# Performance work log

Measured on AMD Instinct MI355X. Metric: run time of the kernel, lower is better.

Reference implementation:

```python
import jax, jax.numpy as jnp
import numpy as np

N = 4096
D_IN = 1024
D_OUT = 1024
NUM_HEADS = 16
HEAD_DIM = D_OUT // NUM_HEADS


def setup_inputs() -> dict:
    key = jax.random.key(0)
    ks = jax.random.split(key, 7)
    scale = 1.0 / np.sqrt(D_IN)
    return {
        "q": jax.random.normal(ks[0], (N, D_IN), dtype=jnp.float32),
        "k": jax.random.normal(ks[1], (N, D_IN), dtype=jnp.float32),
        "v": jax.random.normal(ks[2], (N, D_IN), dtype=jnp.float32),
        "W_q": jax.random.normal(ks[3], (D_IN, D_OUT), dtype=jnp.float32) * scale,
        "W_k": jax.random.normal(ks[4], (D_IN, D_OUT), dtype=jnp.float32) * scale,
        "W_v": jax.random.normal(ks[5], (D_IN, D_OUT), dtype=jnp.float32) * scale,
        "W_o": jax.random.normal(ks[6], (D_OUT, D_OUT), dtype=jnp.float32) * scale,
    }


def reference(q, k, v, W_q, W_k, W_v, W_o):
    n = q.shape[0]
    # QKV projections -> [h, n, d]
    Q = (q @ W_q).reshape(n, NUM_HEADS, HEAD_DIM).transpose(1, 0, 2)
    K = (k @ W_k).reshape(n, NUM_HEADS, HEAD_DIM).transpose(1, 0, 2)
    V = (v @ W_v).reshape(n, NUM_HEADS, HEAD_DIM).transpose(1, 0, 2)
    scores = jnp.einsum('hid,hjd->hij', Q, K) / jnp.sqrt(jnp.float32(HEAD_DIM))
    attn = jax.nn.softmax(scores, axis=-1)  # dropout p=0.0 (eval) -> no-op
    h = jnp.einsum('hij,hjd->hid', attn, V)
    h = h.transpose(1, 0, 2).reshape(n, D_OUT)
    return h @ W_o
```

## Files before the change

kernel.cpp:

```cpp
#include <hip/hip_runtime.h>
#include <math.h>

#define NTOK   4096
#define DMODEL 1024
#define NHEADS 16
#define HDIM   64
#define KDIM   1024

typedef __attribute__((ext_vector_type(8))) short          bf16x8;
typedef __attribute__((ext_vector_type(4))) float          f32x4;
typedef __attribute__((ext_vector_type(4))) unsigned short us4;

static __device__ __forceinline__ unsigned short f2bf(float f) {
    unsigned int u = __float_as_uint(f);
    u += 0x7fffu + ((u >> 16) & 1u);
    return (unsigned short)(u >> 16);
}

static __device__ __forceinline__ unsigned int pk2bf(float a, float b) {
#if __has_builtin(__builtin_amdgcn_cvt_pk_bf16_f32)
    return __builtin_bit_cast(unsigned int,
                              __builtin_amdgcn_cvt_pk_bf16_f32(a, b));
#else
    unsigned int ua = __float_as_uint(a) + 0x8000u;
    unsigned int ub = __float_as_uint(b) + 0x8000u;
    return __builtin_amdgcn_perm(ub, ua, 0x07060302u);
#endif
}

#if __has_builtin(__builtin_amdgcn_exp2f)
#define EXP2(x) __builtin_amdgcn_exp2f(x)
#else
#define EXP2(x) exp2f(x)
#endif

static __device__ __forceinline__ void async_copy16(void* lds, const void* g) {
    __builtin_amdgcn_global_load_lds(
        (const __attribute__((address_space(1))) unsigned int*)g,
        (__attribute__((address_space(3))) unsigned int*)lds, 16, 0, 0);
}

__global__ __launch_bounds__(256)
void cast_wt_kernel(const float* __restrict__ Wq, const float* __restrict__ Wk,
                    const float* __restrict__ Wv, const float* __restrict__ Wo,
                    unsigned short* __restrict__ Tq, unsigned short* __restrict__ Tk,
                    unsigned short* __restrict__ Tv, unsigned short* __restrict__ To) {
    __shared__ float Ws[64][65];
    const float* W;
    unsigned short* T;
    switch (blockIdx.z) {
        case 0:  W = Wq; T = Tq; break;
        case 1:  W = Wk; T = Tk; break;
        case 2:  W = Wv; T = Tv; break;
        default: W = Wo; T = To; break;
    }
    const int k0 = blockIdx.x * 64, n0 = blockIdx.y * 64;
    const int t = threadIdx.x;
    #pragma unroll
    for (int i = 0; i < 4; i++) {
        int c  = i * 256 + t;
        int kk = c >> 4;
        int n4 = (c & 15) << 2;
        *(float4*)(&Ws[kk][n4]) =
            *(const float4*)(W + (size_t)(k0 + kk) * DMODEL + n0 + n4);
    }
    __syncthreads();
    #pragma unroll
    for (int i = 0; i < 4; i++) {
        int c  = i * 256 + t;
        int nn = c >> 4;
        int k4 = (c & 15) << 2;
        us4 o = { f2bf(Ws[k4 + 0][nn]), f2bf(Ws[k4 + 1][nn]),
                  f2bf(Ws[k4 + 2][nn]), f2bf(Ws[k4 + 3][nn]) };
        *(us4*)(T + (size_t)(n0 + nn) * KDIM + k0 + k4) = o;
    }
}

__global__ __launch_bounds__(256)
void cast_in_kernel(const float* __restrict__ q, const float* __restrict__ k,
                    const float* __restrict__ v,
                    unsigned short* __restrict__ Qb,
                    unsigned short* __restrict__ Kb,
                    unsigned short* __restrict__ Vb) {
    const float* src;
    unsigned short* dst;
    switch (blockIdx.y) {
        case 0:  src = q; dst = Qb; break;
        case 1:  src = k; dst = Kb; break;
        default: src = v; dst = Vb; break;
    }
    size_t i = ((size_t)blockIdx.x * 256 + threadIdx.x) * 8;
    float4 f0 = *(const float4*)(src + i);
    float4 f1 = *(const float4*)(src + i + 4);
    uint2 o0 = { pk2bf(f0.x, f0.y), pk2bf(f0.z, f0.w) };
    uint2 o1 = { pk2bf(f1.x, f1.y), pk2bf(f1.z, f1.w) };
    *(uint2*)(dst + i)     = o0;
    *(uint2*)(dst + i + 4) = o1;
}

__global__ __launch_bounds__(256, 3)
void qkv_gemm_pre(const unsigned short* __restrict__ Qb,
                  const unsigned short* __restrict__ Kb,
                  const unsigned short* __restrict__ Vb,
                  const unsigned short* __restrict__ Btq,
                  const unsigned short* __restrict__ Btk,
                  const unsigned short* __restrict__ Btv,
                  unsigned short* __restrict__ Oq, unsigned short* __restrict__ Ok,
                  unsigned short* __restrict__ Ov) {
    __shared__ unsigned short As[128 * 64];
    __shared__ unsigned short Bs[128 * 64];

    const unsigned short* A;
    const unsigned short* Bt;
    unsigned short* Out;
    int mode;
    float sc;
    switch (blockIdx.z) {
        case 0:  A = Qb; Bt = Btq; Out = Oq; mode = 1; sc = 0.18033688011112042f; break;
        case 1:  A = Kb; Bt = Btk; Out = Ok; mode = 1; sc = 1.0f; break;
        default: A = Vb; Bt = Btv; Out = Ov; mode = 2; sc = 1.0f; break;
    }

    const int t    = threadIdx.x;
    const int w    = t >> 6;
    const int lane = t & 63;
    const int quad = lane >> 4;
    const int l15  = lane & 15;
    const int wr   = w >> 1, wc = w & 1;
    const int bm   = blockIdx.y * 128, bn = blockIdx.x * 128;

    f32x4 acc[4][4];
    #pragma unroll
    for (int i = 0; i < 4; i++)
        #pragma unroll
        for (int j = 0; j < 4; j++) acc[i][j] = (f32x4)(0.f);

    for (int k0 = 0; k0 < KDIM; k0 += 64) {
        __syncthreads();
        #pragma unroll
        for (int i = 0; i < 4; i++) {
            int cb = (i * 4 + w) * 64;
            int c  = cb + lane;
            int r  = c >> 3;
            int ko = (c & 7) * 8;
            async_copy16((void*)(Bs + cb * 8),
                         (const void*)(Bt + (size_t)(bn + r) * KDIM + k0 + ko));
            async_copy16((void*)(As + cb * 8),
                         (const void*)(A + (size_t)(bm + r) * KDIM + k0 + ko));
        }
        __syncthreads();
        #pragma unroll
        for (int kq = 0; kq < 2; kq++) {
            bf16x8 af[4], bf[4];
            #pragma unroll
            for (int mt = 0; mt < 4; mt++)
                af[mt] = *(bf16x8*)(As + (wr * 64 + mt * 16 + l15) * 64 + kq * 32 + quad * 8);
            #pragma unroll
            for (int nt = 0; nt < 4; nt++)
                bf[nt] = *(bf16x8*)(Bs + (wc * 64 + nt * 16 + l15) * 64 + kq * 32 + quad * 8);
            #pragma unroll
            for (int mt = 0; mt < 4; mt++)
                #pragma unroll
                for (int nt = 0; nt < 4; nt++)
                    acc[mt][nt] = __builtin_amdgcn_mfma_f32_16x16x32_bf16(
                        af[mt], bf[nt], acc[mt][nt], 0, 0, 0);
        }
    }

    #pragma unroll
    for (int mt = 0; mt < 4; mt++) {
        #pragma unroll
        for (int nt = 0; nt < 4; nt++) {
            int col  = bn + wc * 64 + nt * 16 + l15;
            int row0 = bm + wr * 64 + mt * 16 + quad * 4;
            if (mode == 1) {
                size_t base = ((size_t)(col >> 6)) * NTOK * HDIM + (col & 63);
                #pragma unroll
                for (int r = 0; r < 4; r++)
                    Out[base + (size_t)(row0 + r) * HDIM] = f2bf(acc[mt][nt][r] * sc);
            } else {
                size_t base = ((size_t)(col >> 6)) * HDIM * NTOK +
                              (size_t)(col & 63) * NTOK + row0;
                us4 o = { f2bf(acc[mt][nt][0]), f2bf(acc[mt][nt][1]),
                          f2bf(acc[mt][nt][2]), f2bf(acc[mt][nt][3]) };
                *(us4*)(Out + base) = o;
            }
        }
    }
}

__global__ __launch_bounds__(256, 3)
void qkv_gemm(const float* __restrict__ Aq, const float* __restrict__ Ak,
              const float* __restrict__ Av,
              const unsigned short* __restrict__ Btq,
              const unsigned short* __restrict__ Btk,
              const unsigned short* __restrict__ Btv,
              unsigned short* __restrict__ Oq, unsigned short* __restrict__ Ok,
              unsigned short* __restrict__ Ov) {
    __shared__ unsigned short As[128 * 64];
    __shared__ unsigned short Bs[128 * 64];

    const float* A;
    const unsigned short* Bt;
    unsigned short* Out;
    int mode;
    float sc;
    switch (blockIdx.z) {
        case 0:  A = Aq; Bt = Btq; Out = Oq; mode = 1; sc = 0.18033688011112042f; break;
        case 1:  A = Ak; Bt = Btk; Out = Ok; mode = 1; sc = 1.0f; break;
        default: A = Av; Bt = Btv; Out = Ov; mode = 2; sc = 1.0f; break;
    }

    const int t    = threadIdx.x;
    const int w    = t >> 6;
    const int lane = t & 63;
    const int quad = lane >> 4;
    const int l15  = lane & 15;
    const int wr   = w >> 1, wc = w & 1;
    const int bm   = blockIdx.y * 128, bn = blockIdx.x * 128;

    f32x4 acc[4][4];
    #pragma unroll
    for (int i = 0; i < 4; i++)
        #pragma unroll
        for (int j = 0; j < 4; j++) acc[i][j] = (f32x4)(0.f);

    for (int k0 = 0; k0 < KDIM; k0 += 64) {
        __syncthreads();
        #pragma unroll
        for (int i = 0; i < 4; i++) {
            int cb = (i * 4 + w) * 64;
            int c  = cb + lane;
            int r  = c >> 3;
            int ko = (c & 7) * 8;
            async_copy16((void*)(Bs + cb * 8),
                         (const void*)(Bt + (size_t)(bn + r) * KDIM + k0 + ko));
        }
        #pragma unroll
        for (int i = 0; i < 4; i++) {
            int c2 = i * 256 + t;
            int r  = c2 >> 3;
            int k8 = (c2 & 7) * 8;
            const float* src = A + (size_t)(bm + r) * KDIM + k0 + k8;
            float4 f0 = *(const float4*)(src);
            float4 f1 = *(const float4*)(src + 4);
            uint2 p0 = { pk2bf(f0.x, f0.y), pk2bf(f0.z, f0.w) };
            uint2 p1 = { pk2bf(f1.x, f1.y), pk2bf(f1.z, f1.w) };
            *(uint2*)(As + r * 64 + k8)     = p0;
            *(uint2*)(As + r * 64 + k8 + 4) = p1;
        }
        __syncthreads();
        #pragma unroll
        for (int kq = 0; kq < 2; kq++) {
            bf16x8 af[4], bf[4];
            #pragma unroll
            for (int mt = 0; mt < 4; mt++)
                af[mt] = *(bf16x8*)(As + (wr * 64 + mt * 16 + l15) * 64 + kq * 32 + quad * 8);
            #pragma unroll
            for (int nt = 0; nt < 4; nt++)
                bf[nt] = *(bf16x8*)(Bs + (wc * 64 + nt * 16 + l15) * 64 + kq * 32 + quad * 8);
            #pragma unroll
            for (int mt = 0; mt < 4; mt++)
                #pragma unroll
                for (int nt = 0; nt < 4; nt++)
                    acc[mt][nt] = __builtin_amdgcn_mfma_f32_16x16x32_bf16(
                        af[mt], bf[nt], acc[mt][nt], 0, 0, 0);
        }
    }

    #pragma unroll
    for (int mt = 0; mt < 4; mt++) {
        #pragma unroll
        for (int nt = 0; nt < 4; nt++) {
            int col  = bn + wc * 64 + nt * 16 + l15;
            int row0 = bm + wr * 64 + mt * 16 + quad * 4;
            if (mode == 1) {
                size_t base = ((size_t)(col >> 6)) * NTOK * HDIM + (col & 63);
                #pragma unroll
                for (int r = 0; r < 4; r++)
                    Out[base + (size_t)(row0 + r) * HDIM] = f2bf(acc[mt][nt][r] * sc);
            } else {
                size_t base = ((size_t)(col >> 6)) * HDIM * NTOK +
                              (size_t)(col & 63) * NTOK + row0;
                us4 o = { f2bf(acc[mt][nt][0]), f2bf(acc[mt][nt][1]),
                          f2bf(acc[mt][nt][2]), f2bf(acc[mt][nt][3]) };
                *(us4*)(Out + base) = o;
            }
        }
    }
}

__global__ __launch_bounds__(256, 3)
void out_gemm(const unsigned short* __restrict__ A,
              const unsigned short* __restrict__ Bt,
              float* __restrict__ Out) {
    __shared__ unsigned short As[128 * 64];
    __shared__ unsigned short Bs[128 * 64];

    const int t    = threadIdx.x;
    const int w    = t >> 6;
    const int lane = t & 63;
    const int quad = lane >> 4;
    const int l15  = lane & 15;
    const int wr   = w >> 1, wc = w & 1;
    const int bm   = blockIdx.y * 128, bn = blockIdx.x * 128;

    f32x4 acc[4][4];
    #pragma unroll
    for (int i = 0; i < 4; i++)
        #pragma unroll
        for (int j = 0; j < 4; j++) acc[i][j] = (f32x4)(0.f);

    for (int k0 = 0; k0 < KDIM; k0 += 64) {
        __syncthreads();
        #pragma unroll
        for (int i = 0; i < 4; i++) {
            int cb = (i * 4 + w) * 64;
            int c  = cb + lane;
            int r  = c >> 3;
            int ko = (c & 7) * 8;
            async_copy16((void*)(Bs + cb * 8),
                         (const void*)(Bt + (size_t)(bn + r) * KDIM + k0 + ko));
            async_copy16((void*)(As + cb * 8),
                         (const void*)(A + (size_t)(bm + r) * KDIM + k0 + ko));
        }
        __syncthreads();
        #pragma unroll
        for (int kq = 0; kq < 2; kq++) {
            bf16x8 af[4], bf[4];
            #pragma unroll
            for (int mt = 0; mt < 4; mt++)
                af[mt] = *(bf16x8*)(As + (wr * 64 + mt * 16 + l15) * 64 + kq * 32 + quad * 8);
            #pragma unroll
            for (int nt = 0; nt < 4; nt++)
                bf[nt] = *(bf16x8*)(Bs + (wc * 64 + nt * 16 + l15) * 64 + kq * 32 + quad * 8);
            #pragma unroll
            for (int mt = 0; mt < 4; mt++)
                #pragma unroll
                for (int nt = 0; nt < 4; nt++)
                    acc[mt][nt] = __builtin_amdgcn_mfma_f32_16x16x32_bf16(
                        af[mt], bf[nt], acc[mt][nt], 0, 0, 0);
        }
    }

    #pragma unroll
    for (int mt = 0; mt < 4; mt++) {
        #pragma unroll
        for (int nt = 0; nt < 4; nt++) {
            int col  = bn + wc * 64 + nt * 16 + l15;
            int row0 = bm + wr * 64 + mt * 16 + quad * 4;
            #pragma unroll
            for (int r = 0; r < 4; r++)
                Out[(size_t)(row0 + r) * DMODEL + col] = acc[mt][nt][r];
        }
    }
}

__global__ __launch_bounds__(256)
void attn_mfma(const unsigned short* __restrict__ Q,
               const unsigned short* __restrict__ K,
               const unsigned short* __restrict__ Vt,
               unsigned short* __restrict__ ctx) {
    __shared__ __align__(16) unsigned short Ks[2 * 4096];
    __shared__ __align__(16) unsigned short Vs[2 * 4096];
    __shared__ __align__(16) unsigned short Ps[4][32][72];

    const int h    = blockIdx.y;
    const int qt   = blockIdx.x;
    const int t    = threadIdx.x;
    const int w    = t >> 6;
    const int lane = t & 63;
    const int quad = lane >> 4;
    const int l15  = lane & 15;

    const unsigned short* Qg =
        Q + ((size_t)h * NTOK + qt * 128 + w * 32 + l15) * HDIM;
    bf16x8 qf[2][2];
    qf[0][0] = *(const bf16x8*)(Qg + quad * 8);
    qf[0][1] = *(const bf16x8*)(Qg + 32 + quad * 8);
    qf[1][0] = *(const bf16x8*)(Qg + 16 * HDIM + quad * 8);
    qf[1][1] = *(const bf16x8*)(Qg + 16 * HDIM + 32 + quad * 8);

    const unsigned short* Kg = K  + (size_t)h * NTOK * HDIM;
    const unsigned short* Vg = Vt + (size_t)h * HDIM * NTOK;

    const int rr = t >> 3;
    const int oo = ((t & 7) ^ (rr & 7)) * 8;
    const unsigned short* kbase = Kg + (size_t)rr * HDIM + oo;
    const unsigned short* vbase = Vg + (size_t)rr * NTOK + oo;
    unsigned short* ksd = Ks + w * 512;
    unsigned short* vsd = Vs + w * 512;

    auto stage = [&](int kt, int b) {
        const unsigned short* kp = kbase + (size_t)kt * 64 * HDIM;
        const unsigned short* vp = vbase + kt * 64;
        async_copy16((void*)(ksd + b * 4096),        (const void*)kp);
        async_copy16((void*)(ksd + b * 4096 + 2048), (const void*)(kp + 32 * HDIM));
        async_copy16((void*)(vsd + b * 4096),        (const void*)vp);
        async_copy16((void*)(vsd + b * 4096 + 2048), (const void*)(vp + (size_t)32 * NTOK));
    };

    const int xb = l15 & 7;
    const int a0 = l15 * 64 + ((quad    ) ^ xb) * 8;
    const int a1 = l15 * 64 + ((quad + 4) ^ xb) * 8;

    const bf16x8 ones = { 16256, 16256, 16256, 16256,
                          16256, 16256, 16256, 16256 };

    f32x4 O[2][4];
    f32x4 lacc[2];
    #pragma unroll
    for (int tl = 0; tl < 2; tl++) {
        lacc[tl] = (f32x4)(0.f);
        #pragma unroll
        for (int dt = 0; dt < 4; dt++) O[tl][dt] = (f32x4)(0.f);
    }

    stage(0, 0);

    for (int kt = 0; kt < NTOK / 64; kt++) {
        const int cur = kt & 1;
        __syncthreads();
        if (kt + 1 < NTOK / 64) stage(kt + 1, cur ^ 1);

        f32x4 s[2][4];
        #pragma unroll
        for (int kc = 0; kc < 4; kc++) {
            bf16x8 kf0 = *(bf16x8*)(Ks + cur * 4096 + kc * 1024 + a0);
            bf16x8 kf1 = *(bf16x8*)(Ks + cur * 4096 + kc * 1024 + a1);
            #pragma unroll
            for (int tl = 0; tl < 2; tl++) {
                f32x4 acc = (f32x4)(0.f);
                acc = __builtin_amdgcn_mfma_f32_16x16x32_bf16(kf0, qf[tl][0], acc, 0, 0, 0);
                acc = __builtin_amdgcn_mfma_f32_16x16x32_bf16(kf1, qf[tl][1], acc, 0, 0, 0);
                s[tl][kc] = acc;
            }
        }

        bf16x8 vf[4][2];
        #pragma unroll
        for (int dt = 0; dt < 4; dt++) {
            vf[dt][0] = *(bf16x8*)(Vs + cur * 4096 + dt * 1024 + a0);
            vf[dt][1] = *(bf16x8*)(Vs + cur * 4096 + dt * 1024 + a1);
        }

        #pragma unroll
        for (int tl = 0; tl < 2; tl++) {
            #pragma unroll
            for (int kc = 0; kc < 4; kc++) {
                float e0 = EXP2(s[tl][kc][0]);
                float e1 = EXP2(s[tl][kc][1]);
                float e2 = EXP2(s[tl][kc][2]);
                float e3 = EXP2(s[tl][kc][3]);
                uint2 p = { pk2bf(e0, e1), pk2bf(e2, e3) };
                *(uint2*)(&Ps[w][tl * 16 + l15][kc * 16 + quad * 4]) = p;
            }
            asm volatile("s_waitcnt lgkmcnt(0)" ::: "memory");

            bf16x8 pf0 = *(bf16x8*)(&Ps[w][tl * 16 + l15][quad * 8]);
            bf16x8 pf1 = *(bf16x8*)(&Ps[w][tl * 16 + l15][32 + quad * 8]);
            lacc[tl] = __builtin_amdgcn_mfma_f32_16x16x32_bf16(ones, pf0, lacc[tl], 0, 0, 0);
            lacc[tl] = __builtin_amdgcn_mfma_f32_16x16x32_bf16(ones, pf1, lacc[tl], 0, 0, 0);
            #pragma unroll
            for (int dt = 0; dt < 4; dt++) {
                O[tl][dt] = __builtin_amdgcn_mfma_f32_16x16x32_bf16(vf[dt][0], pf0, O[tl][dt], 0, 0, 0);
                O[tl][dt] = __builtin_amdgcn_mfma_f32_16x16x32_bf16(vf[dt][1], pf1, O[tl][dt], 0, 0, 0);
            }
        }
    }

    #pragma unroll
    for (int tl = 0; tl < 2; tl++) {
        float inv = 1.f / lacc[tl][0];
        size_t row = (size_t)qt * 128 + w * 32 + tl * 16 + l15;
        #pragma unroll
        for (int dt = 0; dt < 4; dt++) {
            uint2 o = { pk2bf(O[tl][dt][0] * inv, O[tl][dt][1] * inv),
                        pk2bf(O[tl][dt][2] * inv, O[tl][dt][3] * inv) };
            *(uint2*)(ctx + row * DMODEL + h * HDIM + dt * 16 + quad * 4) = o;
        }
    }
}

extern "C" void kernel_launch(void* const* d_in, const int* in_sizes, int n_in,
                              void* d_out, int out_size, void* d_ws, size_t ws_size,
                              hipStream_t stream) {
    const float* q  = (const float*)d_in[0];
    const float* k  = (const float*)d_in[1];
    const float* v  = (const float*)d_in[2];
    const float* Wq = (const float*)d_in[3];
    const float* Wk = (const float*)d_in[4];
    const float* Wv = (const float*)d_in[5];
    const float* Wo = (const float*)d_in[6];
    float* out = (float*)d_out;

    unsigned short* WqT = (unsigned short*)d_ws;
    unsigned short* WkT = WqT + (size_t)DMODEL * KDIM;
    unsigned short* WvT = WkT + (size_t)DMODEL * KDIM;
    unsigned short* WoT = WvT + (size_t)DMODEL * KDIM;
    unsigned short* Qh  = WoT + (size_t)DMODEL * KDIM;
    unsigned short* Kh  = Qh  + (size_t)NTOK * DMODEL;
    unsigned short* Vth = Kh  + (size_t)NTOK * DMODEL;
    unsigned short* ctx = Vth + (size_t)NTOK * DMODEL;
    unsigned short* Qb  = ctx + (size_t)NTOK * DMODEL;
    unsigned short* Kb  = Qb  + (size_t)NTOK * DMODEL;
    unsigned short* Vb  = Kb  + (size_t)NTOK * DMODEL;

    const bool precast = ws_size >= (size_t)67108864;

    cast_wt_kernel<<<dim3(16, 16, 4), 256, 0, stream>>>(Wq, Wk, Wv, Wo,
                                                        WqT, WkT, WvT, WoT);
    if (precast) {
        cast_in_kernel<<<dim3(2048, 3), 256, 0, stream>>>(q, k, v, Qb, Kb, Vb);
        qkv_gemm_pre<<<dim3(DMODEL / 128, NTOK / 128, 3), 256, 0, stream>>>(
            Qb, Kb, Vb, WqT, WkT, WvT, Qh, Kh, Vth);
    } else {
        qkv_gemm<<<dim3(DMODEL / 128, NTOK / 128, 3), 256, 0, stream>>>(
            q, k, v, WqT, WkT, WvT, Qh, Kh, Vth);
    }
    attn_mfma<<<dim3(NTOK / 128, NHEADS), 256, 0, stream>>>(Qh, Kh, Vth, ctx);
    out_gemm<<<dim3(DMODEL / 128, NTOK / 128), 256, 0, stream>>>(ctx, WoT, out);
}
```

Before: 277.4 us.

## Load attention K/V fragments directly from global memory and shrink tiles

The attention kernel stops staging K and V tiles through double-buffered shared memory and reads MFMA fragments straight from global (relying on L2/L1 reuse across blocks). Each block now covers 64 query rows instead of 128, with a flattened, head-interleaved grid and occupancy hint 4, so there are more concurrent blocks. The output GEMM tile is halved in M to double its block count. This removes LDS staging and barriers, but every wave now reloads K/V from cache without any intra-block sharing, which increases global/L2 traffic and exposes load latency with no prefetch.

```diff
diff --git a/kernel.cpp b/kernel.cpp
--- a/kernel.cpp
+++ b/kernel.cpp
@@ -294,7 +294,7 @@
 void out_gemm(const unsigned short* __restrict__ A,
               const unsigned short* __restrict__ Bt,
               float* __restrict__ Out) {
-    __shared__ unsigned short As[128 * 64];
+    __shared__ unsigned short As[64 * 64];
     __shared__ unsigned short Bs[128 * 64];
 
     const int t    = threadIdx.x;
@@ -303,11 +303,11 @@
     const int quad = lane >> 4;
     const int l15  = lane & 15;
     const int wr   = w >> 1, wc = w & 1;
-    const int bm   = blockIdx.y * 128, bn = blockIdx.x * 128;
-
-    f32x4 acc[4][4];
-    #pragma unroll
-    for (int i = 0; i < 4; i++)
+    const int bm   = blockIdx.y * 64, bn = blockIdx.x * 128;
+
+    f32x4 acc[2][4];
+    #pragma unroll
+    for (int i = 0; i < 2; i++)
         #pragma unroll
         for (int j = 0; j < 4; j++) acc[i][j] = (f32x4)(0.f);
 
@@ -321,21 +321,28 @@
             int ko = (c & 7) * 8;
             async_copy16((void*)(Bs + cb * 8),
                          (const void*)(Bt + (size_t)(bn + r) * KDIM + k0 + ko));
+        }
+        #pragma unroll
+        for (int i = 0; i < 2; i++) {
+            int cb = (i * 4 + w) * 64;
+            int c  = cb + lane;
+            int r  = c >> 3;
+            int ko = (c & 7) * 8;
             async_copy16((void*)(As + cb * 8),
                          (const void*)(A + (size_t)(bm + r) * KDIM + k0 + ko));
         }
         __syncthreads();
         #pragma unroll
         for (int kq = 0; kq < 2; kq++) {
-            bf16x8 af[4], bf[4];
-            #pragma unroll
-            for (int mt = 0; mt < 4; mt++)
-                af[mt] = *(bf16x8*)(As + (wr * 64 + mt * 16 + l15) * 64 + kq * 32 + quad * 8);
+            bf16x8 af[2], bf[4];
+            #pragma unroll
+            for (int mt = 0; mt < 2; mt++)
+                af[mt] = *(bf16x8*)(As + (wr * 32 + mt * 16 + l15) * 64 + kq * 32 + quad * 8);
             #pragma unroll
             for (int nt = 0; nt < 4; nt++)
                 bf[nt] = *(bf16x8*)(Bs + (wc * 64 + nt * 16 + l15) * 64 + kq * 32 + quad * 8);
             #pragma unroll
-            for (int mt = 0; mt < 4; mt++)
+            for (int mt = 0; mt < 2; mt++)
                 #pragma unroll
                 for (int nt = 0; nt < 4; nt++)
                     acc[mt][nt] = __builtin_amdgcn_mfma_f32_16x16x32_bf16(
@@ -344,11 +351,11 @@
     }
 
     #pragma unroll
-    for (int mt = 0; mt < 4; mt++) {
+    for (int mt = 0; mt < 2; mt++) {
         #pragma unroll
         for (int nt = 0; nt < 4; nt++) {
             int col  = bn + wc * 64 + nt * 16 + l15;
-            int row0 = bm + wr * 64 + mt * 16 + quad * 4;
+            int row0 = bm + wr * 32 + mt * 16 + quad * 4;
             #pragma unroll
             for (int r = 0; r < 4; r++)
                 Out[(size_t)(row0 + r) * DMODEL + col] = acc[mt][nt][r];
@@ -356,17 +363,16 @@
     }
 }
 
-__global__ __launch_bounds__(256)
+__global__ __launch_bounds__(256, 4)
 void attn_mfma(const unsigned short* __restrict__ Q,
                const unsigned short* __restrict__ K,
                const unsigned short* __restrict__ Vt,
                unsigned short* __restrict__ ctx) {
-    __shared__ __align__(16) unsigned short Ks[2 * 4096];
-    __shared__ __align__(16) unsigned short Vs[2 * 4096];
-    __shared__ __align__(16) unsigned short Ps[4][32][72];
-
-    const int h    = blockIdx.y;
-    const int qt   = blockIdx.x;
+    __shared__ __align__(16) unsigned short Ps[4][16][72];
+
+    const int bid  = blockIdx.x;
+    const int h    = bid & 15;
+    const int qt   = bid >> 4;
     const int t    = threadIdx.x;
     const int w    = t >> 6;
     const int lane = t & 63;
@@ -374,111 +380,94 @@
     const int l15  = lane & 15;
 
     const unsigned short* Qg =
-        Q + ((size_t)h * NTOK + qt * 128 + w * 32 + l15) * HDIM;
-    bf16x8 qf[2][2];
-    qf[0][0] = *(const bf16x8*)(Qg + quad * 8);
-    qf[0][1] = *(const bf16x8*)(Qg + 32 + quad * 8);
-    qf[1][0] = *(const bf16x8*)(Qg + 16 * HDIM + quad * 8);
-    qf[1][1] = *(const bf16x8*)(Qg + 16 * HDIM + 32 + quad * 8);
-
-    const unsigned short* Kg = K  + (size_t)h * NTOK * HDIM;
-    const unsigned short* Vg = Vt + (size_t)h * HDIM * NTOK;
-
-    const int rr = t >> 3;
-    const int oo = ((t & 7) ^ (rr & 7)) * 8;
-    const unsigned short* kbase = Kg + (size_t)rr * HDIM + oo;
-    const unsigned short* vbase = Vg + (size_t)rr * NTOK + oo;
-    unsigned short* ksd = Ks + w * 512;
-    unsigned short* vsd = Vs + w * 512;
-
-    auto stage = [&](int kt, int b) {
-        const unsigned short* kp = kbase + (size_t)kt * 64 * HDIM;
-        const unsigned short* vp = vbase + kt * 64;
-        async_copy16((void*)(ksd + b * 4096),        (const void*)kp);
-        async_copy16((void*)(ksd + b * 4096 + 2048), (const void*)(kp + 32 * HDIM));
-        async_copy16((void*)(vsd + b * 4096),        (const void*)vp);
-        async_copy16((void*)(vsd + b * 4096 + 2048), (const void*)(vp + (size_t)32 * NTOK));
-    };
-
-    const int xb = l15 & 7;
-    const int a0 = l15 * 64 + ((quad    ) ^ xb) * 8;
-    const int a1 = l15 * 64 + ((quad + 4) ^ xb) * 8;
+        Q + ((size_t)h * NTOK + qt * 64 + w * 16 + l15) * HDIM;
+    bf16x8 qf0 = *(const bf16x8*)(Qg + quad * 8);
+    bf16x8 qf1 = *(const bf16x8*)(Qg + 32 + quad * 8);
+
+    const unsigned short* kp0 = K + ((size_t)h * NTOK + l15) * HDIM + quad * 8;
+    const unsigned short* kp1 = kp0 + 32 * HDIM;
+    const unsigned short* vp0 = Vt + ((size_t)h * HDIM + l15) * NTOK + quad * 8;
+    const unsigned short* vp1 = vp0 + (size_t)16 * NTOK;
+    const unsigned short* vp2 = vp0 + (size_t)32 * NTOK;
+    const unsigned short* vp3 = vp0 + (size_t)48 * NTOK;
 
     const bf16x8 ones = { 16256, 16256, 16256, 16256,
                           16256, 16256, 16256, 16256 };
 
-    f32x4 O[2][4];
-    f32x4 lacc[2];
-    #pragma unroll
-    for (int tl = 0; tl < 2; tl++) {
-        lacc[tl] = (f32x4)(0.f);
-        #pragma unroll
-        for (int dt = 0; dt < 4; dt++) O[tl][dt] = (f32x4)(0.f);
-    }
-
-    stage(0, 0);
+    f32x4 O[4];
+    f32x4 lacc = (f32x4)(0.f);
+    #pragma unroll
+    for (int dt = 0; dt < 4; dt++) O[dt] = (f32x4)(0.f);
 
     for (int kt = 0; kt < NTOK / 64; kt++) {
-        const int cur = kt & 1;
-        __syncthreads();
-        if (kt + 1 < NTOK / 64) stage(kt + 1, cur ^ 1);
-
-        f32x4 s[2][4];
+        f32x4 s[4];
+        {
+            bf16x8 kf00 = *(const bf16x8*)(kp0);
+            bf16x8 kf01 = *(const bf16x8*)(kp0 + 32);
+            bf16x8 kf10 = *(const bf16x8*)(kp0 + 16 * HDIM);
+            bf16x8 kf11 = *(const bf16x8*)(kp0 + 16 * HDIM + 32);
+            bf16x8 kf20 = *(const bf16x8*)(kp1);
+            bf16x8 kf21 = *(const bf16x8*)(kp1 + 32);
+            bf16x8 kf30 = *(const bf16x8*)(kp1 + 16 * HDIM);
+            bf16x8 kf31 = *(const bf16x8*)(kp1 + 16 * HDIM + 32);
+            f32x4 a0 = (f32x4)(0.f), a1 = (f32x4)(0.f),
+                  a2 = (f32x4)(0.f), a3 = (f32x4)(0.f);
+            a0 = __builtin_amdgcn_mfma_f32_16x16x32_bf16(kf00, qf0, a0, 0, 0, 0);
+            a1 = __builtin_amdgcn_mfma_f32_16x16x32_bf16(kf10, qf0, a1, 0, 0, 0);
+            a2 = __builtin_amdgcn_mfma_f32_16x16x32_bf16(kf20, qf0, a2, 0, 0, 0);
+            a3 = __builtin_amdgcn_mfma_f32_16x16x32_bf16(kf30, qf0, a3, 0, 0, 0);
+            a0 = __builtin_amdgcn_mfma_f32_16x16x32_bf16(kf01, qf1, a0, 0, 0, 0);
+            a1 = __builtin_amdgcn_mfma_f32_16x16x32_bf16(kf11, qf1, a1, 0, 0, 0);
+            a2 = __builtin_amdgcn_mfma_f32_16x16x32_bf16(kf21, qf1, a2, 0, 0, 0);
+            a3 = __builtin_amdgcn_mfma_f32_16x16x32_bf16(kf31, qf1, a3, 0, 0, 0);
+            s[0] = a0; s[1] = a1; s[2] = a2; s[3] = a3;
+        }
+        kp0 += 64 * HDIM;
+        kp1 += 64 * HDIM;
+
+        bf16x8 vf00 = *(const bf16x8*)(vp0);
+        bf16x8 vf01 = *(const bf16x8*)(vp0 + 32);
+        bf16x8 vf10 = *(const bf16x8*)(vp1);
+        bf16x8 vf11 = *(const bf16x8*)(vp1 + 32);
+        bf16x8 vf20 = *(const bf16x8*)(vp2);
+        bf16x8 vf21 = *(const bf16x8*)(vp2 + 32);
+        bf16x8 vf30 = *(const bf16x8*)(vp3);
+        bf16x8 vf31 = *(const bf16x8*)(vp3 + 32);
+        vp0 += 64; vp1 += 64; vp2 += 64; vp3 += 64;
+
         #pragma unroll
         for (int kc = 0; kc < 4; kc++) {
-            bf16x8 kf0 = *(bf16x8*)(Ks + cur * 4096 + kc * 1024 + a0);
-            bf16x8 kf1 = *(bf16x8*)(Ks + cur * 4096 + kc * 1024 + a1);
-            #pragma unroll
-            for (int tl = 0; tl < 2; tl++) {
-                f32x4 acc = (f32x4)(0.f);
-                acc = __builtin_amdgcn_mfma_f32_16x16x32_bf16(kf0, qf[tl][0], acc, 0, 0, 0);
-                acc = __builtin_amdgcn_mfma_f32_16x16x32_bf16(kf1, qf[tl][1], acc, 0, 0, 0);
-                s[tl][kc] = acc;
-            }
-        }
-
-        bf16x8 vf[4][2];
-        #pragma unroll
-        for (int dt = 0; dt < 4; dt++) {
-            vf[dt][0] = *(bf16x8*)(Vs + cur * 4096 + dt * 1024 + a0);
-            vf[dt][1] = *(bf16x8*)(Vs + cur * 4096 + dt * 1024 + a1);
-        }
-
-        #pragma unroll
-        for (int tl = 0; tl < 2; tl++) {
-            #pragma unroll
-            for (int kc = 0; kc < 4; kc++) {
-                float e0 = EXP2(s[tl][kc][0]);
-                float e1 = EXP2(s[tl][kc][1]);
-                float e2 = EXP2(s[tl][kc][2]);
-                float e3 = EXP2(s[tl][kc][3]);
-                uint2 p = { pk2bf(e0, e1), pk2bf(e2, e3) };
-                *(uint2*)(&Ps[w][tl * 16 + l15][kc * 16 + quad * 4]) = p;
-            }
-            asm volatile("s_waitcnt lgkmcnt(0)" ::: "memory");
-
-            bf16x8 pf0 = *(bf16x8*)(&Ps[w][tl * 16 + l15][quad * 8]);
-            bf16x8 pf1 = *(bf16x8*)(&Ps[w][tl * 16 + l15][32 + quad * 8]);
-            lacc[tl] = __builtin_amdgcn_mfma_f32_16x16x32_bf16(ones, pf0, lacc[tl], 0, 0, 0);
-            lacc[tl] = __builtin_amdgcn_mfma_f32_16x16x32_bf16(ones, pf1, lacc[tl], 0, 0, 0);
-            #pragma unroll
-            for (int dt = 0; dt < 4; dt++) {
-                O[tl][dt] = __builtin_amdgcn_mfma_f32_16x16x32_bf16(vf[dt][0], pf0, O[tl][dt], 0, 0, 0);
-                O[tl][dt] = __builtin_amdgcn_mfma_f32_16x16x32_bf16(vf[dt][1], pf1, O[tl][dt], 0, 0, 0);
-            }
-        }
-    }
-
-    #pragma unroll
-    for (int tl = 0; tl < 2; tl++) {
-        float inv = 1.f / lacc[tl][0];
-        size_t row = (size_t)qt * 128 + w * 32 + tl * 16 + l15;
-        #pragma unroll
-        for (int dt = 0; dt < 4; dt++) {
-            uint2 o = { pk2bf(O[tl][dt][0] * inv, O[tl][dt][1] * inv),
-                        pk2bf(O[tl][dt][2] * inv, O[tl][dt][3] * inv) };
-            *(uint2*)(ctx + row * DMODEL + h * HDIM + dt * 16 + quad * 4) = o;
-        }
+            float e0 = EXP2(s[kc][0]);
+            float e1 = EXP2(s[kc][1]);
+            float e2 = EXP2(s[kc][2]);
+            float e3 = EXP2(s[kc][3]);
+            uint2 p = { pk2bf(e0, e1), pk2bf(e2, e3) };
+            *(uint2*)(&Ps[w][l15][kc * 16 + quad * 4]) = p;
+        }
+        asm volatile("s_waitcnt lgkmcnt(0)" ::: "memory");
+
+        bf16x8 pf0 = *(bf16x8*)(&Ps[w][l15][quad * 8]);
+        bf16x8 pf1 = *(bf16x8*)(&Ps[w][l15][32 + quad * 8]);
+
+        lacc  = __builtin_amdgcn_mfma_f32_16x16x32_bf16(ones, pf0, lacc, 0, 0, 0);
+        O[0]  = __builtin_amdgcn_mfma_f32_16x16x32_bf16(vf00, pf0, O[0], 0, 0, 0);
+        O[1]  = __builtin_amdgcn_mfma_f32_16x16x32_bf16(vf10, pf0, O[1], 0, 0, 0);
+        O[2]  = __builtin_amdgcn_mfma_f32_16x16x32_bf16(vf20, pf0, O[2], 0, 0, 0);
+        O[3]  = __builtin_amdgcn_mfma_f32_16x16x32_bf16(vf30, pf0, O[3], 0, 0, 0);
+        lacc  = __builtin_amdgcn_mfma_f32_16x16x32_bf16(ones, pf1, lacc, 0, 0, 0);
+        O[0]  = __builtin_amdgcn_mfma_f32_16x16x32_bf16(vf01, pf1, O[0], 0, 0, 0);
+        O[1]  = __builtin_amdgcn_mfma_f32_16x16x32_bf16(vf11, pf1, O[1], 0, 0, 0);
+        O[2]  = __builtin_amdgcn_mfma_f32_16x16x32_bf16(vf21, pf1, O[2], 0, 0, 0);
+        O[3]  = __builtin_amdgcn_mfma_f32_16x16x32_bf16(vf31, pf1, O[3], 0, 0, 0);
+    }
+
+    float inv = 1.f / lacc[0];
+    size_t row = (size_t)qt * 64 + w * 16 + l15;
+    #pragma unroll
+    for (int dt = 0; dt < 4; dt++) {
+        uint2 o = { pk2bf(O[dt][0] * inv, O[dt][1] * inv),
+                    pk2bf(O[dt][2] * inv, O[dt][3] * inv) };
+        *(uint2*)(ctx + row * DMODEL + h * HDIM + dt * 16 + quad * 4) = o;
     }
 }
 
@@ -518,6 +507,6 @@
         qkv_gemm<<<dim3(DMODEL / 128, NTOK / 128, 3), 256, 0, stream>>>(
             q, k, v, WqT, WkT, WvT, Qh, Kh, Vth);
     }
-    attn_mfma<<<dim3(NTOK / 128, NHEADS), 256, 0, stream>>>(Qh, Kh, Vth, ctx);
-    out_gemm<<<dim3(DMODEL / 128, NTOK / 128), 256, 0, stream>>>(ctx, WoT, out);
-}
+    attn_mfma<<<dim3(NTOK / 64 * NHEADS), 256, 0, stream>>>(Qh, Kh, Vth, ctx);
+    out_gemm<<<dim3(DMODEL / 128, NTOK / 64), 256, 0, stream>>>(ctx, WoT, out);
+}
```

Measured after the change: 611.6 us. 2.2x slower.

## Split attention KV range across two blocks with combine pass; shrink out_gemm M-tile

Applied to the files above, without the earlier changes.

Attention is split along the key dimension into two halves, each computed by its own block. Each half writes unnormalized bf16 partial outputs and row sums, and a separate combine kernel adds the halves and normalizes. This doubles the number of attention blocks to improve CU occupancy, at the cost of extra global traffic and one more launch. The output GEMM tile is reduced from 128 to 64 rows, doubling its grid for better load balance at the price of less B-tile reuse.

```diff
diff --git a/kernel.cpp b/kernel.cpp
--- a/kernel.cpp
+++ b/kernel.cpp
@@ -294,7 +294,7 @@
 void out_gemm(const unsigned short* __restrict__ A,
               const unsigned short* __restrict__ Bt,
               float* __restrict__ Out) {
-    __shared__ unsigned short As[128 * 64];
+    __shared__ unsigned short As[64 * 64];
     __shared__ unsigned short Bs[128 * 64];
 
     const int t    = threadIdx.x;
@@ -303,11 +303,11 @@
     const int quad = lane >> 4;
     const int l15  = lane & 15;
     const int wr   = w >> 1, wc = w & 1;
-    const int bm   = blockIdx.y * 128, bn = blockIdx.x * 128;
-
-    f32x4 acc[4][4];
-    #pragma unroll
-    for (int i = 0; i < 4; i++)
+    const int bm   = blockIdx.y * 64, bn = blockIdx.x * 128;
+
+    f32x4 acc[2][4];
+    #pragma unroll
+    for (int i = 0; i < 2; i++)
         #pragma unroll
         for (int j = 0; j < 4; j++) acc[i][j] = (f32x4)(0.f);
 
@@ -321,21 +321,28 @@
             int ko = (c & 7) * 8;
             async_copy16((void*)(Bs + cb * 8),
                          (const void*)(Bt + (size_t)(bn + r) * KDIM + k0 + ko));
+        }
+        #pragma unroll
+        for (int i = 0; i < 2; i++) {
+            int cb = (i * 4 + w) * 64;
+            int c  = cb + lane;
+            int r  = c >> 3;
+            int ko = (c & 7) * 8;
             async_copy16((void*)(As + cb * 8),
                          (const void*)(A + (size_t)(bm + r) * KDIM + k0 + ko));
         }
         __syncthreads();
         #pragma unroll
         for (int kq = 0; kq < 2; kq++) {
-            bf16x8 af[4], bf[4];
-            #pragma unroll
-            for (int mt = 0; mt < 4; mt++)
-                af[mt] = *(bf16x8*)(As + (wr * 64 + mt * 16 + l15) * 64 + kq * 32 + quad * 8);
+            bf16x8 af[2], bf[4];
+            #pragma unroll
+            for (int mt = 0; mt < 2; mt++)
+                af[mt] = *(bf16x8*)(As + (wr * 32 + mt * 16 + l15) * 64 + kq * 32 + quad * 8);
             #pragma unroll
             for (int nt = 0; nt < 4; nt++)
                 bf[nt] = *(bf16x8*)(Bs + (wc * 64 + nt * 16 + l15) * 64 + kq * 32 + quad * 8);
             #pragma unroll
-            for (int mt = 0; mt < 4; mt++)
+            for (int mt = 0; mt < 2; mt++)
                 #pragma unroll
                 for (int nt = 0; nt < 4; nt++)
                     acc[mt][nt] = __builtin_amdgcn_mfma_f32_16x16x32_bf16(
@@ -344,16 +351,166 @@
     }
 
     #pragma unroll
-    for (int mt = 0; mt < 4; mt++) {
+    for (int mt = 0; mt < 2; mt++) {
         #pragma unroll
         for (int nt = 0; nt < 4; nt++) {
             int col  = bn + wc * 64 + nt * 16 + l15;
-            int row0 = bm + wr * 64 + mt * 16 + quad * 4;
+            int row0 = bm + wr * 32 + mt * 16 + quad * 4;
             #pragma unroll
             for (int r = 0; r < 4; r++)
                 Out[(size_t)(row0 + r) * DMODEL + col] = acc[mt][nt][r];
         }
     }
+}
+
+__global__ __launch_bounds__(256, 4)
+void attn_split(const unsigned short* __restrict__ Q,
+                const unsigned short* __restrict__ K,
+                const unsigned short* __restrict__ Vt,
+                unsigned short* __restrict__ PO,
+                float* __restrict__ lbuf) {
+    __shared__ __align__(16) unsigned short Ks[4096];
+    __shared__ __align__(16) unsigned short Vs[4096];
+    __shared__ __align__(16) unsigned short Ps[4][16][72];
+
+    const int qt   = blockIdx.x;
+    const int h    = blockIdx.y;
+    const int half = blockIdx.z;
+    const int t    = threadIdx.x;
+    const int w    = t >> 6;
+    const int lane = t & 63;
+    const int quad = lane >> 4;
+    const int l15  = lane & 15;
+
+    const unsigned short* Qg =
+        Q + ((size_t)h * NTOK + qt * 128 + w * 32 + l15) * HDIM;
+    bf16x8 qf[2][2];
+    qf[0][0] = *(const bf16x8*)(Qg + quad * 8);
+    qf[0][1] = *(const bf16x8*)(Qg + 32 + quad * 8);
+    qf[1][0] = *(const bf16x8*)(Qg + 16 * HDIM + quad * 8);
+    qf[1][1] = *(const bf16x8*)(Qg + 16 * HDIM + 32 + quad * 8);
+
+    const unsigned short* Kg = K  + ((size_t)h * NTOK + half * 2048) * HDIM;
+    const unsigned short* Vg = Vt + (size_t)h * HDIM * NTOK + half * 2048;
+
+    const int rr = t >> 3;
+    const int oo = ((t & 7) ^ (rr & 7)) * 8;
+    const unsigned short* kbase = Kg + (size_t)rr * HDIM + oo;
+    const unsigned short* vbase = Vg + (size_t)rr * NTOK + oo;
+    unsigned short* ksd = Ks + w * 512;
+    unsigned short* vsd = Vs + w * 512;
+
+    const int xb = l15 & 7;
+    const int a0 = l15 * 64 + ((quad    ) ^ xb) * 8;
+    const int a1 = l15 * 64 + ((quad + 4) ^ xb) * 8;
+
+    const bf16x8 ones = { 16256, 16256, 16256, 16256,
+                          16256, 16256, 16256, 16256 };
+
+    f32x4 O[2][4];
+    f32x4 lacc[2];
+    #pragma unroll
+    for (int tl = 0; tl < 2; tl++) {
+        lacc[tl] = (f32x4)(0.f);
+        #pragma unroll
+        for (int dt = 0; dt < 4; dt++) O[tl][dt] = (f32x4)(0.f);
+    }
+
+    for (int kt = 0; kt < 32; kt++) {
+        __syncthreads();
+        {
+            const unsigned short* kp = kbase + (size_t)kt * 64 * HDIM;
+            const unsigned short* vp = vbase + kt * 64;
+            async_copy16((void*)(ksd),        (const void*)kp);
+            async_copy16((void*)(ksd + 2048), (const void*)(kp + 32 * HDIM));
+            async_copy16((void*)(vsd),        (const void*)vp);
+            async_copy16((void*)(vsd + 2048), (const void*)(vp + (size_t)32 * NTOK));
+        }
+        __syncthreads();
+
+        f32x4 s[2][4];
+        #pragma unroll
+        for (int kc = 0; kc < 4; kc++) {
+            bf16x8 kf0 = *(bf16x8*)(Ks + kc * 1024 + a0);
+            bf16x8 kf1 = *(bf16x8*)(Ks + kc * 1024 + a1);
+            #pragma unroll
+            for (int tl = 0; tl < 2; tl++) {
+                f32x4 acc = (f32x4)(0.f);
+                acc = __builtin_amdgcn_mfma_f32_16x16x32_bf16(kf0, qf[tl][0], acc, 0, 0, 0);
+                acc = __builtin_amdgcn_mfma_f32_16x16x32_bf16(kf1, qf[tl][1], acc, 0, 0, 0);
+                s[tl][kc] = acc;
+            }
+        }
+
+        bf16x8 vf[4][2];
+        #pragma unroll
+        for (int dt = 0; dt < 4; dt++) {
+            vf[dt][0] = *(bf16x8*)(Vs + dt * 1024 + a0);
+            vf[dt][1] = *(bf16x8*)(Vs + dt * 1024 + a1);
+        }
+
+        #pragma unroll
+        for (int tl = 0; tl < 2; tl++) {
+            #pragma unroll
+            for (int kc = 0; kc < 4; kc++) {
+                float e0 = EXP2(s[tl][kc][0]);
+                float e1 = EXP2(s[tl][kc][1]);
+                float e2 = EXP2(s[tl][kc][2]);
+                float e3 = EXP2(s[tl][kc][3]);
+                uint2 p = { pk2bf(e0, e1), pk2bf(e2, e3) };
+                *(uint2*)(&Ps[w][l15][kc * 16 + quad * 4]) = p;
+            }
+            asm volatile("s_waitcnt lgkmcnt(0)" ::: "memory");
+
+            bf16x8 pf0 = *(bf16x8*)(&Ps[w][l15][quad * 8]);
+            bf16x8 pf1 = *(bf16x8*)(&Ps[w][l15][32 + quad * 8]);
+            lacc[tl] = __builtin_amdgcn_mfma_f32_16x16x32_bf16(ones, pf0, lacc[tl], 0, 0, 0);
+            lacc[tl] = __builtin_amdgcn_mfma_f32_16x16x32_bf16(ones, pf1, lacc[tl], 0, 0, 0);
+            #pragma unroll
+            for (int dt = 0; dt < 4; dt++) {
+                O[tl][dt] = __builtin_amdgcn_mfma_f32_16x16x32_bf16(vf[dt][0], pf0, O[tl][dt], 0, 0, 0);
+                O[tl][dt] = __builtin_amdgcn_mfma_f32_16x16x32_bf16(vf[dt][1], pf1, O[tl][dt], 0, 0, 0);
+            }
+        }
+    }
+
+    unsigned short* POh = PO + (size_t)half * NTOK * DMODEL;
+    #pragma unroll
+    for (int tl = 0; tl < 2; tl++) {
+        size_t row = (size_t)qt * 128 + w * 32 + tl * 16 + l15;
+        #pragma unroll
+        for (int dt = 0; dt < 4; dt++) {
+            uint2 o = { pk2bf(O[tl][dt][0], O[tl][dt][1]),
+                        pk2bf(O[tl][dt][2], O[tl][dt][3]) };
+            *(uint2*)(POh + row * DMODEL + h * HDIM + dt * 16 + quad * 4) = o;
+        }
+        if (quad == 0)
+            lbuf[((size_t)half * NHEADS + h) * NTOK + row] = lacc[tl][0];
+    }
+}
+
+__global__ __launch_bounds__(256)
+void combine_kernel(const unsigned short* __restrict__ PO,
+                    const float* __restrict__ lbuf,
+                    unsigned short* __restrict__ ctx) {
+    size_t idx = ((size_t)blockIdx.x * 256 + threadIdx.x) * 8;
+    int row = (int)(idx >> 10);
+    int c   = (int)(idx & 1023);
+    int h   = c >> 6;
+    uint4 a = *(const uint4*)(PO + idx);
+    uint4 b = *(const uint4*)(PO + (size_t)NTOK * DMODEL + idx);
+    float la = lbuf[(size_t)h * NTOK + row];
+    float lb = lbuf[(size_t)NHEADS * NTOK + (size_t)h * NTOK + row];
+    float inv = 1.f / (la + lb);
+    auto comb = [&](unsigned int x, unsigned int y) -> unsigned int {
+        float x0 = __uint_as_float(x << 16);
+        float x1 = __uint_as_float(x & 0xffff0000u);
+        float y0 = __uint_as_float(y << 16);
+        float y1 = __uint_as_float(y & 0xffff0000u);
+        return pk2bf((x0 + y0) * inv, (x1 + y1) * inv);
+    };
+    uint4 o = { comb(a.x, b.x), comb(a.y, b.y), comb(a.z, b.z), comb(a.w, b.w) };
+    *(uint4*)(ctx + idx) = o;
 }
 
 __global__ __launch_bounds__(256)
@@ -505,19 +662,25 @@
     unsigned short* Qb  = ctx + (size_t)NTOK * DMODEL;
     unsigned short* Kb  = Qb  + (size_t)NTOK * DMODEL;
     unsigned short* Vb  = Kb  + (size_t)NTOK * DMODEL;
-
-    const bool precast = ws_size >= (size_t)67108864;
+    unsigned short* PO  = Qb;
+    float*          lb  = (float*)(PO + (size_t)2 * NTOK * DMODEL);
+
+    const bool bigws = ws_size >= (size_t)67108864;
 
     cast_wt_kernel<<<dim3(16, 16, 4), 256, 0, stream>>>(Wq, Wk, Wv, Wo,
                                                         WqT, WkT, WvT, WoT);
-    if (precast) {
+    if (bigws) {
         cast_in_kernel<<<dim3(2048, 3), 256, 0, stream>>>(q, k, v, Qb, Kb, Vb);
         qkv_gemm_pre<<<dim3(DMODEL / 128, NTOK / 128, 3), 256, 0, stream>>>(
             Qb, Kb, Vb, WqT, WkT, WvT, Qh, Kh, Vth);
+        attn_split<<<dim3(NTOK / 128, NHEADS, 2), 256, 0, stream>>>(
+            Qh, Kh, Vth, PO, lb);
+        combine_kernel<<<dim3(NTOK * DMODEL / 8 / 256), 256, 0, stream>>>(
+            PO, lb, ctx);
     } else {
         qkv_gemm<<<dim3(DMODEL / 128, NTOK / 128, 3), 256, 0, stream>>>(
             q, k, v, WqT, WkT, WvT, Qh, Kh, Vth);
-    }
-    attn_mfma<<<dim3(NTOK / 128, NHEADS), 256, 0, stream>>>(Qh, Kh, Vth, ctx);
-    out_gemm<<<dim3(DMODEL / 128, NTOK / 128), 256, 0, stream>>>(ctx, WoT, out);
-}
+        attn_mfma<<<dim3(NTOK / 128, NHEADS), 256, 0, stream>>>(Qh, Kh, Vth, ctx);
+    }
+    out_gemm<<<dim3(DMODEL / 128, NTOK / 64), 256, 0, stream>>>(ctx, WoT, out);
+}
```

New measurement: 256.0 us. 7.7% less time.
